# Performance work log

Hardware: AMD Instinct MI355X
Metric: run time of the kernel (lower is better)

Reference implementation:

```python
import jax, jax.numpy as jnp
import numpy as np
import math

T, N, D, H = 1024, 8, 1024, 16
HD = D // H  # head_dim = 64


def setup_inputs() -> dict:
    key = jax.random.key(0)
    k1, k2, k3, k4 = jax.random.split(key, 4)
    scale = 1.0 / math.sqrt(D)  # roughly xavier-scale params
    return {
        "x": jax.random.normal(k1, (T, N, D), dtype=jnp.float32),
        "q_weight": jax.random.normal(k2, (D, H, HD), dtype=jnp.float32) * scale,
        "v_weight": jax.random.normal(k3, (D, H, HD), dtype=jnp.float32) * scale,
        "out_w": jax.random.normal(k4, (D, D), dtype=jnp.float32) * scale,
        "out_b": jnp.zeros((D,), dtype=jnp.float32),
    }


def reference(x, q_weight, v_weight, out_w, out_b):
    inv_sqrt_hd = 1.0 / math.sqrt(HD)
    # q = k : (T, N, H, HD)
    q = jnp.einsum('tbm,mhd->tbhd', x, q_weight)
    q_sq = jnp.einsum('tbhd,tbhd->tbh', q, q)  # squared norms
    # squared L2 distance logits: (T, S, N, H)
    squared_dist = q_sq[:, None] + q_sq[None, :] - 2.0 * jnp.einsum('tbhd,sbhd->tsbh', q, q)
    attn_logits = -squared_dist * inv_sqrt_hd
    attn_weights = jax.nn.softmax(attn_logits, axis=1)  # softmax over source dim S
    # A = W_q W_q^T per head: (H, D, D)
    A = jnp.einsum('mhd,nhd->hmn', q_weight, q_weight) * inv_sqrt_hd
    XA = jnp.einsum('tbm,hmn->tbhn', x, A)           # (T, N, H, D)
    PXA = jnp.einsum('tsbh,sbhm->tbhm', attn_weights, XA)  # (T, N, H, D)
    PXAV = jnp.einsum('tbhm,mhd->tbhd', PXA, v_weight).reshape(T, N, D)
    return PXAV @ out_w.T + out_b
```

## Files before the change

kernel.cpp:

```cpp
#include <hip/hip_runtime.h>
#include <hip/hip_bf16.h>

#define T_ 1024
#define N_ 8
#define D_ 1024
#define H_ 16
#define HD_ 64

typedef __attribute__((ext_vector_type(8))) short bf16x8;
typedef __attribute__((ext_vector_type(4))) float f32x4;
typedef __attribute__((ext_vector_type(16))) float f32x16;
typedef __attribute__((ext_vector_type(4))) int i32x4;
typedef __attribute__((ext_vector_type(2))) int i32x2;
typedef unsigned short u16;
typedef unsigned int u32;

__device__ __forceinline__ float bf2f(u16 u){
  union { float f; unsigned int i; } v; v.i = ((unsigned int)u) << 16; return v.f;
}
__device__ __forceinline__ u16 f2bf(float f){
  union { float f; unsigned int i; } v; v.f = f;
  unsigned int r = v.i + 0x7FFFu + ((v.i >> 16) & 1u);
  return (u16)(r >> 16);
}
__device__ __forceinline__ u16 f2bf_fast(float f){
  __hip_bfloat16 h = __float2bfloat16(f);
  return *reinterpret_cast<u16*>(&h);
}
__device__ __forceinline__ float exp2_raw(float x){
  float r;
  asm("v_exp_f32 %0, %1" : "=v"(r) : "v"(x));
  return r;
}
__device__ __forceinline__ void gl_lds16(const u16* g, u16* l){
  __builtin_amdgcn_global_load_lds(
      (const __attribute__((address_space(1))) unsigned int*)g,
      (__attribute__((address_space(3))) unsigned int*)(unsigned int)(unsigned long long)l,
      16, 0, 0);
}
__device__ __forceinline__ void gl_lds4(const float* g, float* l){
  __builtin_amdgcn_global_load_lds(
      (const __attribute__((address_space(1))) unsigned int*)g,
      (__attribute__((address_space(3))) unsigned int*)(unsigned int)(unsigned long long)l,
      4, 0, 0);
}

__global__ __launch_bounds__(256) void k_wqt(const float* __restrict__ Wq, u16* __restrict__ Wqt){
  __shared__ float tld[64][65];
  int m0 = blockIdx.x * 64, n0 = blockIdx.y * 64;
  int col = threadIdx.x & 63, rq = threadIdx.x >> 6;
  #pragma unroll
  for (int p = 0; p < 16; ++p){
    int row = rq * 16 + p;
    tld[row][col] = Wq[(size_t)(m0 + row) * D_ + n0 + col];
  }
  __syncthreads();
  #pragma unroll
  for (int p = 0; p < 16; ++p){
    int row = rq * 16 + p;
    Wqt[(size_t)(n0 + row) * D_ + m0 + col] = f2bf(tld[col][row]);
  }
}

__global__ __launch_bounds__(256) void k_bmatp(const float* __restrict__ qw, const float* __restrict__ vw,
                                               float* __restrict__ Bp){
  int h = (int)blockIdx.x >> 3, sp = (int)blockIdx.x & 7;
  int tid = threadIdx.x, lane = tid & 63, w = tid >> 6;
  int g = lane >> 4, c = lane & 15;
  __shared__ u16 Qt[64 * 72];
  __shared__ u16 Vt[64 * 72];
  f32x4 zero = {0.f, 0.f, 0.f, 0.f};
  f32x4 acc[4];
  #pragma unroll
  for (int eb = 0; eb < 4; ++eb) acc[eb] = zero;
  int m = tid >> 2, cg = tid & 3;
  for (int mt = sp * 128; mt < sp * 128 + 128; mt += 64){
    __syncthreads();
    #pragma unroll
    for (int q = 0; q < 4; ++q){
      int e0 = cg * 16 + q * 4;
      f32x4 vq = *(const f32x4*)(qw + (size_t)(mt + m) * D_ + h * 64 + e0);
      f32x4 vv = *(const f32x4*)(vw + (size_t)(mt + m) * D_ + h * 64 + e0);
      #pragma unroll
      for (int j = 0; j < 4; ++j){
        Qt[(e0 + j) * 72 + m] = f2bf_fast(vq[j]);
        Vt[(e0 + j) * 72 + m] = f2bf_fast(vv[j]);
      }
    }
    __syncthreads();
    #pragma unroll
    for (int kk = 0; kk < 2; ++kk){
      bf16x8 av = *(const bf16x8*)&Vt[(w * 16 + c) * 72 + kk * 32 + g * 8];
      #pragma unroll
      for (int eb = 0; eb < 4; ++eb){
        bf16x8 bq = *(const bf16x8*)&Qt[(eb * 16 + c) * 72 + kk * 32 + g * 8];
        acc[eb] = __builtin_amdgcn_mfma_f32_16x16x32_bf16(av, bq, acc[eb], 0, 0, 0);
      }
    }
  }
  #pragma unroll
  for (int eb = 0; eb < 4; ++eb)
    #pragma unroll
    for (int r = 0; r < 4; ++r){
      int d = w * 16 + g * 4 + r, e = eb * 16 + c;
      Bp[(((size_t)sp * 16 + h) * 64 + d) * 64 + e] = acc[eb][r];
    }
}

__global__ __launch_bounds__(256) void k_bred(const float* __restrict__ Bp, u16* __restrict__ Bt){
  int i = blockIdx.x * 256 + threadIdx.x;
  float s = 0.f;
  #pragma unroll
  for (int j = 0; j < 8; ++j) s += Bp[(size_t)j * 65536 + i];
  Bt[i] = f2bf(s * 0.125f);
}

__device__ __forceinline__ int swz(int row, int colbyte){
  return row * 64 + (((colbyte) ^ ((row & 7) << 4)) >> 1);
}

template<int A_F32, int B_F32, int EPI>
__global__ __launch_bounds__(256) void k_gemm(const void* __restrict__ A_, const void* __restrict__ B_,
                                              void* __restrict__ Cv, const float* __restrict__ bias,
                                              int M, int N, int K){
  int nbn = N >> 7;
  int ii = (int)blockIdx.x;
  int sw = (ii & 7) * 64 + (ii >> 3);
  int bm = sw / nbn, bn = sw % nbn;
  int tid = threadIdx.x, lane = tid & 63, wid = tid >> 6;
  int wr = wid >> 1, wc = wid & 1, g = lane >> 4, c = lane & 15;
  __shared__ u16 As[128 * 64];
  __shared__ u16 Bs[128 * 64];
  f32x4 zero = {0.f, 0.f, 0.f, 0.f};
  f32x4 acc[4][4];
  #pragma unroll
  for (int m = 0; m < 4; ++m)
    #pragma unroll
    for (int n = 0; n < 4; ++n) acc[m][n] = zero;
  for (int kt = 0; kt < K; kt += 64){
    __syncthreads();
    #pragma unroll
    for (int p = 0; p < 4; ++p){
      int ci = tid + p * 256;
      int row = ci >> 3, c8 = ci & 7;
      int dst = swz(row, c8 * 16);
      if (A_F32){
        const float* A = (const float*)A_;
        const float* src = A + (size_t)(bm * 128 + row) * K + kt + c8 * 8;
        f32x4 v0 = *(const f32x4*)src;
        f32x4 v1 = *(const f32x4*)(src + 4);
        union { u16 u[8]; i32x4 v; } pk;
        #pragma unroll
        for (int j = 0; j < 4; ++j){ pk.u[j] = f2bf_fast(v0[j]); pk.u[4 + j] = f2bf_fast(v1[j]); }
        *(i32x4*)&As[dst] = pk.v;
      } else {
        const u16* A = (const u16*)A_;
        *(i32x4*)&As[dst] = *(const i32x4*)(A + (size_t)(bm * 128 + row) * K + kt + c8 * 8);
      }
      if (B_F32){
        const float* B = (const float*)B_;
        const float* src = B + (size_t)(bn * 128 + row) * K + kt + c8 * 8;
        f32x4 v0 = *(const f32x4*)src;
        f32x4 v1 = *(const f32x4*)(src + 4);
        union { u16 u[8]; i32x4 v; } pk;
        #pragma unroll
        for (int j = 0; j < 4; ++j){ pk.u[j] = f2bf_fast(v0[j]); pk.u[4 + j] = f2bf_fast(v1[j]); }
        *(i32x4*)&Bs[dst] = pk.v;
      } else {
        const u16* B = (const u16*)B_;
        *(i32x4*)&Bs[dst] = *(const i32x4*)(B + (size_t)(bn * 128 + row) * K + kt + c8 * 8);
      }
    }
    __syncthreads();
    #pragma unroll
    for (int kk = 0; kk < 2; ++kk){
      bf16x8 af[4], bfr[4];
      #pragma unroll
      for (int m = 0; m < 4; ++m){
        int row = wr * 64 + m * 16 + c;
        af[m] = *(const bf16x8*)&As[swz(row, kk * 64 + g * 16)];
      }
      #pragma unroll
      for (int n = 0; n < 4; ++n){
        int row = wc * 64 + n * 16 + c;
        bfr[n] = *(const bf16x8*)&Bs[swz(row, kk * 64 + g * 16)];
      }
      #pragma unroll
      for (int m = 0; m < 4; ++m)
        #pragma unroll
        for (int n = 0; n < 4; ++n)
          acc[m][n] = __builtin_amdgcn_mfma_f32_16x16x32_bf16(af[m], bfr[n], acc[m][n], 0, 0, 0);
    }
  }
  #pragma unroll
  for (int m = 0; m < 4; ++m)
    #pragma unroll
    for (int n = 0; n < 4; ++n)
      #pragma unroll
      for (int r = 0; r < 4; ++r){
        int row = bm * 128 + wr * 64 + m * 16 + g * 4 + r;
        int col = bn * 128 + wc * 64 + n * 16 + c;
        float v = acc[m][n][r];
        if (EPI == 0){
          int t = row >> 3, b = row & 7, hh = col >> 6, dd = col & 63;
          ((u16*)Cv)[(((size_t)(b * H_ + hh)) * T_ + t) * HD_ + dd] = f2bf(v);
        } else {
          ((float*)Cv)[(size_t)row * N + col] = v + bias[col];
        }
      }
}

__global__ __launch_bounds__(64) void k_u(const u16* __restrict__ qb, const u16* __restrict__ Bt,
                                          u16* __restrict__ ubt, float* __restrict__ qsq){
  int bh = blockIdx.x >> 4, tt = blockIdx.x & 15;
  int h = bh & 15, t0 = tt * 64;
  int lane = threadIdx.x, g = lane >> 4, c = lane & 15;
  const float QS_SCALE = 0.125f * 1.44269504088896340736f;
  bf16x8 af[4][2], bq[4][2];
  #pragma unroll
  for (int mf = 0; mf < 4; ++mf)
    #pragma unroll
    for (int kk = 0; kk < 2; ++kk)
      af[mf][kk] = *(const bf16x8*)(Bt + ((size_t)(h * 64 + mf * 16 + c)) * 64 + kk * 32 + g * 8);
  #pragma unroll
  for (int nf = 0; nf < 4; ++nf)
    #pragma unroll
    for (int kk = 0; kk < 2; ++kk)
      bq[nf][kk] = *(const bf16x8*)(qb + ((size_t)(bh * 1024 + t0 + nf * 16 + c)) * 64 + kk * 32 + g * 8);
  #pragma unroll
  for (int nf = 0; nf < 4; ++nf){
    float ss = 0.f;
    #pragma unroll
    for (int kk = 0; kk < 2; ++kk)
      #pragma unroll
      for (int j = 0; j < 8; ++j){ float f = bf2f((u16)bq[nf][kk][j]); ss = fmaf(f, f, ss); }
    ss += __shfl_xor(ss, 16);
    ss += __shfl_xor(ss, 32);
    if (lane < 16) qsq[(size_t)bh * 1024 + t0 + nf * 16 + lane] = ss * QS_SCALE;
  }
  f32x4 zero = {0.f, 0.f, 0.f, 0.f};
  f32x4 acc[4][4];
  #pragma unroll
  for (int mf = 0; mf < 4; ++mf)
    #pragma unroll
    for (int nf = 0; nf < 4; ++nf) acc[mf][nf] = zero;
  #pragma unroll
  for (int kk = 0; kk < 2; ++kk)
    #pragma unroll
    for (int mf = 0; mf < 4; ++mf)
      #pragma unroll
      for (int nf = 0; nf < 4; ++nf)
        acc[mf][nf] = __builtin_amdgcn_mfma_f32_16x16x32_bf16(af[mf][kk], bq[nf][kk], acc[mf][nf], 0, 0, 0);
  #pragma unroll
  for (int mf = 0; mf < 4; ++mf)
    #pragma unroll
    for (int nf = 0; nf < 4; ++nf)
      #pragma unroll
      for (int r = 0; r < 4; ++r)
        ubt[((size_t)(bh * 64 + mf * 16 + g * 4 + r)) * 1024 + t0 + nf * 16 + c] = f2bf(acc[mf][nf][r]);
}

__global__ __launch_bounds__(256, 4) void k_attn(const u16* __restrict__ qb, const u16* __restrict__ ubt,
                                                 const float* __restrict__ qsq, u16* __restrict__ obm){
  int i = (int)blockIdx.x;
  int bh = ((i & 7) << 4) + (i >> 6);
  int tt = (i >> 3) & 7;
  int b = bh >> 4, h = bh & 15;
  int tid = threadIdx.x, w = tid >> 6, lane = tid & 63;
  int lo = lane & 31, hi = lane >> 5;
  __shared__ u16 Kl[64 * 64];
  __shared__ u16 Ul[64 * 64];
  __shared__ float Qs[64];
  const float C1 = 0.25f * 1.44269504088896340736f;
  int t0 = tt * 128 + w * 32;
  const u16* qbh = qb + (size_t)bh * 65536;
  const u16* ubh = ubt + (size_t)bh * 65536;
  const float* qsb = qsq + (size_t)bh * 1024;
  bf16x8 qB[4];
  #pragma unroll
  for (int kd = 0; kd < 4; ++kd)
    qB[kd] = *(const bf16x8*)(qbh + (t0 + lo) * 64 + kd * 16 + hi * 8);
  f32x16 o0 = {0,0,0,0,0,0,0,0,0,0,0,0,0,0,0,0};
  f32x16 o1 = {0,0,0,0,0,0,0,0,0,0,0,0,0,0,0,0};
  const f32x16 zero16 = {0,0,0,0,0,0,0,0,0,0,0,0,0,0,0,0};
  float l_c = 0.f;
  int slot0 = (w * 2 + 0) * 64 + lane, slot1 = (w * 2 + 1) * 64 + lane;
  int r0 = slot0 >> 3, sc0 = ((slot0 & 7) ^ (r0 & 7)) * 8;
  int r1 = slot1 >> 3, sc1 = ((slot1 & 7) ^ (r1 & 7)) * 8;
  u16* kD0 = &Kl[(w * 2 + 0) * 512];
  u16* kD1 = &Kl[(w * 2 + 1) * 512];
  u16* uD0 = &Ul[(w * 2 + 0) * 512];
  u16* uD1 = &Ul[(w * 2 + 1) * 512];
  for (int st = 0; st < 16; ++st){
    int s0 = st * 64;
    __syncthreads();
    gl_lds16(qbh + (s0 + r0) * 64 + sc0, kD0);
    gl_lds16(qbh + (s0 + r1) * 64 + sc1, kD1);
    gl_lds16(ubh + (size_t)r0 * 1024 + s0 + sc0, uD0);
    gl_lds16(ubh + (size_t)r1 * 1024 + s0 + sc1, uD1);
    if (w == 0) gl_lds4(qsb + s0 + lane, &Qs[0]);
    __syncthreads();
    #pragma unroll
    for (int ts = 0; ts < 2; ++ts){
      f32x16 sf = zero16;
      __builtin_amdgcn_s_setprio(1);
      #pragma unroll
      for (int kd = 0; kd < 4; ++kd){
        bf16x8 kA = *(const bf16x8*)&Kl[swz(ts * 32 + lo, kd * 32 + hi * 16)];
        sf = __builtin_amdgcn_mfma_f32_32x32x16_bf16(kA, qB[kd], sf, 0, 0, 0);
      }
      __builtin_amdgcn_s_setprio(0);
      f32x4 qs_[4];
      #pragma unroll
      for (int q = 0; q < 4; ++q)
        qs_[q] = *(const f32x4*)&Qs[ts * 32 + q * 8 + hi * 4];
      float p[16];
      #pragma unroll
      for (int r = 0; r < 16; ++r)
        p[r] = exp2_raw(fmaf(sf[r], C1, -qs_[r >> 2][r & 3]));
      float sA = ((p[0] + p[1]) + (p[2] + p[3])) + ((p[4] + p[5]) + (p[6] + p[7]));
      float sB = ((p[8] + p[9]) + (p[10] + p[11])) + ((p[12] + p[13]) + (p[14] + p[15]));
      l_c += sA + sB;
      u32 W[8];
      #pragma unroll
      for (int q = 0; q < 8; ++q)
        W[q] = ((u32)f2bf_fast(p[2 * q + 1]) << 16) | (u32)f2bf_fast(p[2 * q]);
      #pragma unroll
      for (int ml = 0; ml < 2; ++ml){
        int m_g = ts * 2 + ml;
        int base = ml * 4;
        i32x2 sw0 = __builtin_amdgcn_permlane32_swap((int)W[base + 0], (int)W[base + 2], false, false);
        i32x2 sw1 = __builtin_amdgcn_permlane32_swap((int)W[base + 1], (int)W[base + 3], false, false);
        union { u32 wd[4]; bf16x8 v; } pa;
        pa.wd[0] = (u32)sw0[0]; pa.wd[1] = (u32)sw1[0]; pa.wd[2] = (u32)sw0[1]; pa.wd[3] = (u32)sw1[1];
        bf16x8 u0 = *(const bf16x8*)&Ul[swz(lo, m_g * 32 + hi * 16)];
        bf16x8 u1 = *(const bf16x8*)&Ul[swz(32 + lo, m_g * 32 + hi * 16)];
        __builtin_amdgcn_s_setprio(1);
        o0 = __builtin_amdgcn_mfma_f32_32x32x16_bf16(pa.v, u0, o0, 0, 0, 0);
        o1 = __builtin_amdgcn_mfma_f32_32x32x16_bf16(pa.v, u1, o1, 0, 0, 0);
        __builtin_amdgcn_s_setprio(0);
      }
    }
  }
  l_c += __shfl_xor(l_c, 32);
  float inv = 1.0f / l_c;
  #pragma unroll
  for (int r = 0; r < 16; ++r){
    int tr = (r & 3) + 8 * (r >> 2) + 4 * hi;
    float invr = __shfl(inv, tr);
    size_t rowb = ((size_t)((t0 + tr) * 8 + b)) * 1024 + h * 64;
    obm[rowb + lo] = f2bf(o0[r] * invr);
    obm[rowb + 32 + lo] = f2bf(o1[r] * invr);
  }
}

extern "C" void kernel_launch(void* const* d_in, const int* in_sizes, int n_in,
                              void* d_out, int out_size, void* d_ws, size_t ws_size,
                              hipStream_t stream) {
  const float* x   = (const float*)d_in[0];
  const float* qw  = (const float*)d_in[1];
  const float* vw  = (const float*)d_in[2];
  const float* ow  = (const float*)d_in[3];
  const float* ob_bias = (const float*)d_in[4];
  float* out = (float*)d_out;

  float* Bp = (float*)d_out;
  u16* qb  = (u16*)d_out;
  u16* ubt = (u16*)((char*)d_out + (size_t)16 * 1024 * 1024);

  char* ws = (char*)d_ws;
  size_t off = 0;
  auto alloc = [&](size_t bytes) -> void* {
    void* p = ws + off;
    off += (bytes + 255) & ~(size_t)255;
    return p;
  };
  u16*   wqt = (u16*)  alloc((size_t)1024 * 1024 * 2);
  u16*   obm = (u16*)  alloc((size_t)8192 * 1024 * 2);
  float* qsq = (float*)alloc((size_t)128 * 1024 * 4);
  u16*   Bt  = (u16*)  alloc((size_t)16 * 64 * 64 * 2);

  k_bmatp<<<128, 256, 0, stream>>>(qw, vw, Bp);
  k_bred<<<256, 256, 0, stream>>>(Bp, Bt);
  k_wqt<<<dim3(16, 16), 256, 0, stream>>>(qw, wqt);
  k_gemm<1, 0, 0><<<512, 256, 0, stream>>>(x, wqt, qb, nullptr, 8192, 1024, 1024);
  k_u<<<2048, 64, 0, stream>>>(qb, Bt, ubt, qsq);
  k_attn<<<1024, 256, 0, stream>>>(qb, ubt, qsq, obm);
  k_gemm<0, 1, 1><<<512, 256, 0, stream>>>(obm, ow, out, ob_bias, 8192, 1024, 1024);
}
```

Before: 141.8 us.

## Double-buffer K/U tiles and preload all query norms in attention kernel

The attention kernel now keeps two LDS buffers for the K and U tiles. It issues the global-to-LDS loads for the next source tile before computing on the current one, which drops one barrier per iteration and overlaps memory traffic with MFMA work. The full 1024-entry squared-norm vector for the head is loaded into LDS once at kernel start, replacing the per-iteration 4-byte DMA load. LDS use per block roughly doubles, which could limit how many blocks fit on a CU.

```diff
diff --git a/kernel.cpp b/kernel.cpp
--- a/kernel.cpp
+++ b/kernel.cpp
@@ -37,12 +37,6 @@
       (const __attribute__((address_space(1))) unsigned int*)g,
       (__attribute__((address_space(3))) unsigned int*)(unsigned int)(unsigned long long)l,
       16, 0, 0);
-}
-__device__ __forceinline__ void gl_lds4(const float* g, float* l){
-  __builtin_amdgcn_global_load_lds(
-      (const __attribute__((address_space(1))) unsigned int*)g,
-      (__attribute__((address_space(3))) unsigned int*)(unsigned int)(unsigned long long)l,
-      4, 0, 0);
 }
 
 __global__ __launch_bounds__(256) void k_wqt(const float* __restrict__ Wq, u16* __restrict__ Wqt){
@@ -268,14 +262,15 @@
   int b = bh >> 4, h = bh & 15;
   int tid = threadIdx.x, w = tid >> 6, lane = tid & 63;
   int lo = lane & 31, hi = lane >> 5;
-  __shared__ u16 Kl[64 * 64];
-  __shared__ u16 Ul[64 * 64];
-  __shared__ float Qs[64];
+  __shared__ u16 Kl[2][64 * 64];
+  __shared__ u16 Ul[2][64 * 64];
+  __shared__ float Qs[1024];
   const float C1 = 0.25f * 1.44269504088896340736f;
   int t0 = tt * 128 + w * 32;
   const u16* qbh = qb + (size_t)bh * 65536;
   const u16* ubh = ubt + (size_t)bh * 65536;
   const float* qsb = qsq + (size_t)bh * 1024;
+  *(f32x4*)&Qs[tid * 4] = *(const f32x4*)(qsb + tid * 4);
   bf16x8 qB[4];
   #pragma unroll
   for (int kd = 0; kd < 4; ++kd)
@@ -287,33 +282,39 @@
   int slot0 = (w * 2 + 0) * 64 + lane, slot1 = (w * 2 + 1) * 64 + lane;
   int r0 = slot0 >> 3, sc0 = ((slot0 & 7) ^ (r0 & 7)) * 8;
   int r1 = slot1 >> 3, sc1 = ((slot1 & 7) ^ (r1 & 7)) * 8;
-  u16* kD0 = &Kl[(w * 2 + 0) * 512];
-  u16* kD1 = &Kl[(w * 2 + 1) * 512];
-  u16* uD0 = &Ul[(w * 2 + 0) * 512];
-  u16* uD1 = &Ul[(w * 2 + 1) * 512];
+  int d0 = (w * 2 + 0) * 512, d1 = (w * 2 + 1) * 512;
+  gl_lds16(qbh + r0 * 64 + sc0, &Kl[0][d0]);
+  gl_lds16(qbh + r1 * 64 + sc1, &Kl[0][d1]);
+  gl_lds16(ubh + (size_t)r0 * 1024 + sc0, &Ul[0][d0]);
+  gl_lds16(ubh + (size_t)r1 * 1024 + sc1, &Ul[0][d1]);
+  int cur = 0;
   for (int st = 0; st < 16; ++st){
     int s0 = st * 64;
     __syncthreads();
-    gl_lds16(qbh + (s0 + r0) * 64 + sc0, kD0);
-    gl_lds16(qbh + (s0 + r1) * 64 + sc1, kD1);
-    gl_lds16(ubh + (size_t)r0 * 1024 + s0 + sc0, uD0);
-    gl_lds16(ubh + (size_t)r1 * 1024 + s0 + sc1, uD1);
-    if (w == 0) gl_lds4(qsb + s0 + lane, &Qs[0]);
-    __syncthreads();
+    if (st < 15){
+      int s1 = s0 + 64;
+      int nb = cur ^ 1;
+      gl_lds16(qbh + (s1 + r0) * 64 + sc0, &Kl[nb][d0]);
+      gl_lds16(qbh + (s1 + r1) * 64 + sc1, &Kl[nb][d1]);
+      gl_lds16(ubh + (size_t)r0 * 1024 + s1 + sc0, &Ul[nb][d0]);
+      gl_lds16(ubh + (size_t)r1 * 1024 + s1 + sc1, &Ul[nb][d1]);
+    }
+    const u16* Kc = &Kl[cur][0];
+    const u16* Uc = &Ul[cur][0];
     #pragma unroll
     for (int ts = 0; ts < 2; ++ts){
       f32x16 sf = zero16;
       __builtin_amdgcn_s_setprio(1);
       #pragma unroll
       for (int kd = 0; kd < 4; ++kd){
-        bf16x8 kA = *(const bf16x8*)&Kl[swz(ts * 32 + lo, kd * 32 + hi * 16)];
+        bf16x8 kA = *(const bf16x8*)&Kc[swz(ts * 32 + lo, kd * 32 + hi * 16)];
         sf = __builtin_amdgcn_mfma_f32_32x32x16_bf16(kA, qB[kd], sf, 0, 0, 0);
       }
       __builtin_amdgcn_s_setprio(0);
       f32x4 qs_[4];
       #pragma unroll
       for (int q = 0; q < 4; ++q)
-        qs_[q] = *(const f32x4*)&Qs[ts * 32 + q * 8 + hi * 4];
+        qs_[q] = *(const f32x4*)&Qs[s0 + ts * 32 + q * 8 + hi * 4];
       float p[16];
       #pragma unroll
       for (int r = 0; r < 16; ++r)
@@ -333,14 +334,15 @@
         i32x2 sw1 = __builtin_amdgcn_permlane32_swap((int)W[base + 1], (int)W[base + 3], false, false);
         union { u32 wd[4]; bf16x8 v; } pa;
         pa.wd[0] = (u32)sw0[0]; pa.wd[1] = (u32)sw1[0]; pa.wd[2] = (u32)sw0[1]; pa.wd[3] = (u32)sw1[1];
-        bf16x8 u0 = *(const bf16x8*)&Ul[swz(lo, m_g * 32 + hi * 16)];
-        bf16x8 u1 = *(const bf16x8*)&Ul[swz(32 + lo, m_g * 32 + hi * 16)];
+        bf16x8 u0 = *(const bf16x8*)&Uc[swz(lo, m_g * 32 + hi * 16)];
+        bf16x8 u1 = *(const bf16x8*)&Uc[swz(32 + lo, m_g * 32 + hi * 16)];
         __builtin_amdgcn_s_setprio(1);
         o0 = __builtin_amdgcn_mfma_f32_32x32x16_bf16(pa.v, u0, o0, 0, 0, 0);
         o1 = __builtin_amdgcn_mfma_f32_32x32x16_bf16(pa.v, u1, o1, 0, 0, 0);
         __builtin_amdgcn_s_setprio(0);
       }
     }
+    cur ^= 1;
   }
   l_c += __shfl_xor(l_c, 32);
   float inv = 1.0f / l_c;
```

Result: faster. 136.1 us (-4.1%).
